# Performance work log

Hardware: AMD Instinct MI355X
Metric: run time of the kernel (lower is better)

## Reference

```python
import jax, jax.numpy as jnp
import numpy as np

NH = 12        # main attention heads (head_dim = 64)
SNH = 4        # scorer self-attention heads
ALPHA = 0.1    # static survival-score weight
EPS = 1e-8


def _linear(x, w, b):
    # torch nn.Linear: y = x @ W^T + b
    return x @ w.T + b


def _mha(x, in_w, in_b, out_w, out_b, n_heads, maskf):
    # torch nn.MultiheadAttention (batch_first, eval mode)
    B, S, D = x.shape
    hd = D // n_heads
    qkv = _linear(x, in_w, in_b)                      # [B,S,3D]
    q, k, v = jnp.split(qkv, 3, axis=-1)
    sp = lambda t: t.reshape(B, S, n_heads, hd).transpose(0, 2, 1, 3)
    q, k, v = sp(q), sp(k), sp(v)                     # [B,h,S,hd]
    scores = jnp.einsum('bhqd,bhkd->bhqk', q, k) / jnp.asarray(np.sqrt(hd), x.dtype)
    scores = jnp.where(maskf[:, None, None, :] > 0, scores, jnp.asarray(-1e9, x.dtype))
    aw = jax.nn.softmax(scores, axis=-1)
    o = jnp.einsum('bhqk,bhkd->bhqd', aw, v).transpose(0, 2, 1, 3).reshape(B, S, D)
    return _linear(o, out_w, out_b)


def _survival_scores(x, maskf, sp_w, sp_b, sa_in_w, sa_in_b, sa_out_w, sa_out_b,
                     nw1, nb1, nw2, nb2, mw1, mb1, mw2, mb2, dw1, db1, dw2, db2):
    h = _linear(x, sp_w, sp_b)                        # [B,S,256]
    h = _mha(h, sa_in_w, sa_in_b, sa_out_w, sa_out_b, SNH, maskf)
    n = jax.nn.softplus(_linear(jax.nn.relu(_linear(h, nw1, nb1)), nw2, nb2))[..., 0]
    mu = jax.nn.sigmoid(_linear(jax.nn.relu(_linear(h, mw1, mb1)), mw2, mb2))[..., 0]
    delta = jax.nn.relu(_linear(jax.nn.relu(_linear(h, dw1, db1)), dw2, db2))[..., 0]
    # S = log(N) + log(mu / mu_c) - delta, with mu_c = 1.0
    return jnp.log(n + EPS) + jnp.log(mu + EPS) - delta


def setup_inputs() -> dict:
    key = jax.random.key(0)
    ks = iter(jax.random.split(key, 40))
    W = lambda shape: jax.random.normal(next(ks), shape, jnp.float32) * 0.05
    Z = lambda shape: jnp.zeros(shape, jnp.float32)
    B, S, H, I = 2, 2048, 768, 256
    inp = {
        'x': jax.random.normal(next(ks), (B, S, H), jnp.float32),
        'mask': jnp.ones((B, S), jnp.int32),
        'qw': W((H, H)), 'qb': Z((H,)),
        'kw': W((H, H)), 'kb': Z((H,)),
        'vw': W((H, H)), 'vb': Z((H,)),
        'ow': W((H, H)), 'ob': Z((H,)),
        'sp_w': W((I, H)), 'sp_b': Z((I,)),
        'sa_in_w': W((3 * I, I)), 'sa_in_b': Z((3 * I,)),
        'sa_out_w': W((I, I)), 'sa_out_b': Z((I,)),
        'nw1': W((I // 2, I)), 'nb1': Z((I // 2,)), 'nw2': W((1, I // 2)), 'nb2': Z((1,)),
        'mw1': W((I // 2, I)), 'mb1': Z((I // 2,)), 'mw2': W((1, I // 2)), 'mb2': Z((1,)),
        'dw1': W((I // 2, I)), 'db1': Z((I // 2,)), 'dw2': W((1, I // 2)), 'db2': Z((1,)),
    }
    return inp


def reference(x, mask, qw, qb, kw, kb, vw, vb, ow, ob,
              sp_w, sp_b, sa_in_w, sa_in_b, sa_out_w, sa_out_b,
              nw1, nb1, nw2, nb2, mw1, mb1, mw2, mb2, dw1, db1, dw2, db2):
    B, S, H = x.shape
    hd = H // NH
    maskf = mask.astype(x.dtype)
    # Q/K/V projections -> [B,h,S,hd]
    sp = lambda t: t.reshape(B, S, NH, hd).transpose(0, 2, 1, 3)
    q = sp(_linear(x, qw, qb))
    k = sp(_linear(x, kw, kb))
    v = sp(_linear(x, vw, vb))
    scores = jnp.einsum('bhqd,bhkd->bhqk', q, k) / jnp.asarray(np.sqrt(hd), x.dtype)
    # survival-score bias (broadcast over heads and query positions)
    surv = _survival_scores(x, maskf, sp_w, sp_b, sa_in_w, sa_in_b, sa_out_w, sa_out_b,
                            nw1, nb1, nw2, nb2, mw1, mb1, mw2, mb2, dw1, db1, dw2, db2)
    scores = scores + ALPHA * surv[:, None, None, :]
    scores = scores + (1.0 - maskf)[:, None, None, :] * -1e9
    aw = jax.nn.softmax(scores, axis=-1)
    out = jnp.einsum('bhqk,bhkd->bhqd', aw, v).transpose(0, 2, 1, 3).reshape(B, S, H)
    return _linear(out, ow, ob)
```

## Files before the change

### kernel.cpp

```cpp
#include <hip/hip_runtime.h>
#include <math.h>

typedef __bf16 bf16;
typedef __bf16 bfrag __attribute__((ext_vector_type(8)));
typedef __bf16 bf4 __attribute__((ext_vector_type(4)));
typedef float f4 __attribute__((ext_vector_type(4)));
typedef float f16v __attribute__((ext_vector_type(16)));

#define LOG2E 1.4426950408889634f

#define DEV static __device__ __forceinline__

DEV f4 MFMA(bfrag a, bfrag b, f4 c) {
  return __builtin_amdgcn_mfma_f32_16x16x32_bf16(a, b, c, 0, 0, 0);
}
DEV f16v MFMA32(bfrag a, bfrag b, f16v c) {
  return __builtin_amdgcn_mfma_f32_32x32x16_bf16(a, b, c, 0, 0, 0);
}
DEV float ex2(float x) { return __builtin_amdgcn_exp2f(x); }
DEV unsigned pkbf(float a, float b) {
  bf16 ha = (bf16)a, hb = (bf16)b;
  unsigned short ua = __builtin_bit_cast(unsigned short, ha);
  unsigned short ub = __builtin_bit_cast(unsigned short, hb);
  return (unsigned)ua | ((unsigned)ub << 16);
}
DEV void gload_lds16(const bf16* g, bf16* l) {
  __builtin_amdgcn_global_load_lds(
      (const __attribute__((address_space(1))) void*)g,
      (__attribute__((address_space(3))) void*)l, 16, 0, 0);
}

__global__ __launch_bounds__(256) void pack_all(
    const float* __restrict__ x, const float* __restrict__ qw, const float* __restrict__ kw,
    const float* __restrict__ vw, const float* __restrict__ ow, const float* __restrict__ sp_w,
    const float* __restrict__ sa_in_w, const float* __restrict__ sa_out_w,
    const float* __restrict__ nw1, const float* __restrict__ mw1, const float* __restrict__ dw1,
    const float* __restrict__ qb, const float* __restrict__ kb, const float* __restrict__ vb,
    const float* __restrict__ nb1, const float* __restrict__ mb1, const float* __restrict__ db1,
    const int* __restrict__ mask,
    bf16* __restrict__ xb, bf16* __restrict__ wqkv, bf16* __restrict__ wob,
    bf16* __restrict__ spwb, bf16* __restrict__ sainb, bf16* __restrict__ saoutb,
    bf16* __restrict__ w1pack, float* __restrict__ bqkv, float* __restrict__ b1pack,
    float* __restrict__ maskBias) {
  int bid = blockIdx.x;
  int tid = threadIdx.x;
  const float* src = nullptr;
  bf16* dst = nullptr;
  int rel = 0;
  if (bid < 3072)      { src = x;       dst = xb;                   rel = bid; }
  else if (bid < 3648) { src = qw;      dst = wqkv;                 rel = bid - 3072; }
  else if (bid < 4224) { src = kw;      dst = wqkv + 589824;        rel = bid - 3648; }
  else if (bid < 4800) { src = vw;      dst = wqkv + 2 * 589824;    rel = bid - 4224; }
  else if (bid < 5376) { src = ow;      dst = wob;                  rel = bid - 4800; }
  else if (bid < 5568) { src = sp_w;    dst = spwb;                 rel = bid - 5376; }
  else if (bid < 5760) { src = sa_in_w; dst = sainb;                rel = bid - 5568; }
  else if (bid < 5824) { src = sa_out_w;dst = saoutb;               rel = bid - 5760; }
  else if (bid < 5856) { src = nw1;     dst = w1pack;               rel = bid - 5824; }
  else if (bid < 5888) { src = mw1;     dst = w1pack + 32768;       rel = bid - 5856; }
  else if (bid < 5920) { src = dw1;     dst = w1pack + 2 * 32768;   rel = bid - 5888; }
  else if (bid == 5920) {
    if (tid < 576) {
      int which = tid / 192, j = tid % 192;
      const float* s = which == 0 ? qb : (which == 1 ? kb : vb);
      reinterpret_cast<float4*>(bqkv)[tid] = reinterpret_cast<const float4*>(s)[j];
    }
    return;
  } else if (bid == 5921) {
    if (tid < 96) {
      int which = tid / 32, j = tid % 32;
      const float* s = which == 0 ? nb1 : (which == 1 ? mb1 : db1);
      reinterpret_cast<float4*>(b1pack)[tid] = reinterpret_cast<const float4*>(s)[j];
    }
    return;
  } else {
    int idx = (bid - 5922) * 256 + tid;
    int4 m = reinterpret_cast<const int4*>(mask)[idx];
    float4 o;
    o.x = m.x > 0 ? 0.f : -1e9f * LOG2E;
    o.y = m.y > 0 ? 0.f : -1e9f * LOG2E;
    o.z = m.z > 0 ? 0.f : -1e9f * LOG2E;
    o.w = m.w > 0 ? 0.f : -1e9f * LOG2E;
    reinterpret_cast<float4*>(maskBias)[idx] = o;
    return;
  }
  int i = rel * 256 + tid;
  float4 v = reinterpret_cast<const float4*>(src)[i];
  bf4 o;
  o[0] = (bf16)v.x; o[1] = (bf16)v.y; o[2] = (bf16)v.z; o[3] = (bf16)v.w;
  reinterpret_cast<bf4*>(dst)[i] = o;
}

template<int OUTF32, int RELU>
__global__ __launch_bounds__(256) void gemm_nt(
    const bf16* __restrict__ A, int lda,
    const bf16* __restrict__ W, int ldw,
    const float* __restrict__ bias,
    void* __restrict__ C, int ldc,
    int N64, int K) {
  int lane = threadIdx.x & 63;
  int w = threadIdx.x >> 6;
  int lrow = lane & 15, lgrp = lane >> 4;
  int tn = blockIdx.x % N64, tm = blockIdx.x / N64;
  int m0 = tm * 64 + (w >> 1) * 32;
  int n0 = tn * 64 + (w & 1) * 32;
  const bf16* Ab = A + (size_t)m0 * lda + lgrp * 8;
  const bf16* Wb = W + (size_t)n0 * ldw + lgrp * 8;
  f4 acc[2][2] = {};
  for (int k0 = 0; k0 < K; k0 += 32) {
    bfrag a0 = *(const bfrag*)(Ab + (size_t)lrow * lda + k0);
    bfrag a1 = *(const bfrag*)(Ab + (size_t)(lrow + 16) * lda + k0);
    bfrag b0 = *(const bfrag*)(Wb + (size_t)lrow * ldw + k0);
    bfrag b1 = *(const bfrag*)(Wb + (size_t)(lrow + 16) * ldw + k0);
    acc[0][0] = MFMA(a0, b0, acc[0][0]);
    acc[0][1] = MFMA(a0, b1, acc[0][1]);
    acc[1][0] = MFMA(a1, b0, acc[1][0]);
    acc[1][1] = MFMA(a1, b1, acc[1][1]);
  }
#pragma unroll
  for (int mi = 0; mi < 2; mi++)
#pragma unroll
    for (int nj = 0; nj < 2; nj++) {
      int col = n0 + nj * 16 + lrow;
      float bv = bias[col];
      int rowb = m0 + mi * 16 + lgrp * 4;
#pragma unroll
      for (int i = 0; i < 4; i++) {
        float v = acc[mi][nj][i] + bv;
        if (RELU) v = fmaxf(v, 0.f);
        if (OUTF32)
          ((float*)C)[(size_t)(rowb + i) * ldc + col] = v;
        else
          ((bf16*)C)[(size_t)(rowb + i) * ldc + col] = (bf16)v;
      }
    }
}

template<int OUTF32>
__global__ __launch_bounds__(256, 2) void gemm_big(
    const bf16* __restrict__ A,
    const bf16* __restrict__ W,
    const float* __restrict__ bias,
    void* __restrict__ C, int ldc,
    int N128, int K) {
  __shared__ char smem[65536];
  int lane = threadIdx.x & 63;
  int w = threadIdx.x >> 6;
  int lrow = lane & 15, lgrp = lane >> 4;
  int tn = blockIdx.x % N128, tm = blockIdx.x / N128;
  int m0 = tm * 128, n0 = tn * 128;

  int srow = lane >> 3;
  int sslot = (lane & 7) ^ srow;

  auto stage = [&](int bufb, int k0) {
#pragma unroll
    for (int j = 0; j < 4; j++) {
      int rb = (w * 4 + j) * 8 + srow;
      gload_lds16(A + (size_t)(m0 + rb) * K + k0 + sslot * 8,
                  (bf16*)(smem + bufb + (w * 4 + j) * 1024));
      gload_lds16(W + (size_t)(n0 + rb) * K + k0 + sslot * 8,
                  (bf16*)(smem + bufb + 16384 + (w * 4 + j) * 1024));
    }
  };

  f4 acc[4][4] = {};
  int swz = (lrow & 7) << 4;
  int mbase = (w >> 1) * 64, nbase = (w & 1) * 64;

  stage(0, 0);
  __syncthreads();
  int buf = 0;
  int nt = K / 64;
  for (int t = 0; t < nt; t++) {
    int nbuf = buf ^ 32768;
    if (t + 1 < nt) stage(nbuf, (t + 1) * 64);
    const char* As = smem + buf;
    const char* Ws = smem + buf + 16384;
#pragma unroll
    for (int kb = 0; kb < 128; kb += 64) {
      bfrag a[4], b[4];
#pragma unroll
      for (int i = 0; i < 4; i++) {
        a[i] = *(const bfrag*)(As + (mbase + i * 16 + lrow) * 128 + ((kb + lgrp * 16) ^ swz));
        b[i] = *(const bfrag*)(Ws + (nbase + i * 16 + lrow) * 128 + ((kb + lgrp * 16) ^ swz));
      }
#pragma unroll
      for (int mi = 0; mi < 4; mi++)
#pragma unroll
        for (int nj = 0; nj < 4; nj++)
          acc[mi][nj] = MFMA(a[mi], b[nj], acc[mi][nj]);
    }
    __syncthreads();
    buf = nbuf;
  }

#pragma unroll
  for (int mi = 0; mi < 4; mi++)
#pragma unroll
    for (int nj = 0; nj < 4; nj++) {
      int col = n0 + nbase + nj * 16 + lrow;
      float bv = bias[col];
      int rowb = m0 + mbase + mi * 16 + lgrp * 4;
#pragma unroll
      for (int i = 0; i < 4; i++) {
        float v = acc[mi][nj][i] + bv;
        if (OUTF32)
          ((float*)C)[(size_t)(rowb + i) * ldc + col] = v;
        else
          ((bf16*)C)[(size_t)(rowb + i) * ldc + col] = (bf16)v;
      }
    }
}

__global__ __launch_bounds__(256) void vtrans(const bf16* __restrict__ V, int rs, int coff,
                                              bf16* __restrict__ Vt, int H, int S) {
  int nst = S / 64;
  int st = blockIdx.x % nst;
  int h = (blockIdx.x / nst) % H;
  int b = blockIdx.x / (nst * H);
  __shared__ bf16 tile[64][72];
  int t = threadIdx.x;
  int r = t >> 2, c = t & 3;
  const bf16* src = V + ((size_t)b * S + st * 64 + r) * rs + coff + h * 64 + c * 16;
  bfrag v0 = *(const bfrag*)(src);
  bfrag v1 = *(const bfrag*)(src + 8);
  *(bfrag*)&tile[r][c * 16] = v0;
  *(bfrag*)&tile[r][c * 16 + 8] = v1;
  __syncthreads();
  bf16* dst = Vt + (((size_t)b * H + h) * 64 + r) * S + st * 64 + c * 16;
  bfrag o0, o1;
#pragma unroll
  for (int j = 0; j < 8; j++) {
    o0[j] = tile[c * 16 + j][r];
    o1[j] = tile[c * 16 + 8 + j][r];
  }
  *(bfrag*)dst = o0;
  *(bfrag*)(dst + 8) = o1;
}

template<int SPLIT, int PARTIAL>
__global__ __launch_bounds__(256) void flash6_k(
    const bf16* __restrict__ Q, const bf16* __restrict__ Kp, int rs,
    const bf16* __restrict__ Vt, const float* __restrict__ bias,
    bf16* __restrict__ O, int ors,
    float* __restrict__ Opart, float* __restrict__ Lpart,
    int H, int S, float scale, int Bc) {
  int nqt = S / 128;
  int bid = blockIdx.x;
  int qt = bid % nqt;
  int hh = (bid / nqt) % H;
  int b = (bid / (nqt * H)) % Bc;
  int sp = bid / (nqt * H * Bc);
  int lane = threadIdx.x & 63, w = threadIdx.x >> 6;
  int l31 = lane & 31, hf = lane >> 5;
  int q0 = qt * 128 + w * 32;
  const int kchunk = S / SPLIT;
  int k_beg = sp * kchunk;
  int swzl = (l31 & 7) << 4;

  const bf16* Qb = Q + ((size_t)b * S + q0 + l31) * rs + hh * 64 + hf * 8;
  bfrag qf[4];
#pragma unroll
  for (int c = 0; c < 4; c++) qf[c] = *(const bfrag*)(Qb + 16 * c);

  const bf16* gK0 = Kp + ((size_t)b * S + k_beg) * rs + hh * 64;
  const bf16* gV0 = Vt + (((size_t)b * H + hh) * 64) * (size_t)S + k_beg;
  const float* biasb = bias + (size_t)b * S;

  __shared__ bf16 KT[2][4096];
  __shared__ bf16 VT[2][4096];

  f16v acc0, acc1;
#pragma unroll
  for (int r = 0; r < 16; r++) { acc0[r] = 0.f; acc1[r] = 0.f; }
  float lrun = 0.f;

  int sidx0 = (w * 2) * 64 + lane;
  int sidx1 = (w * 2 + 1) * 64 + lane;
  int srow0 = sidx0 >> 3, sc0 = sidx0 & 7;
  int srow1 = sidx1 >> 3, sc1 = sidx1 & 7;
  int soff0 = srow0 * 128 + ((sc0 * 16) ^ ((srow0 & 7) << 4));
  int soff1 = srow1 * 128 + ((sc1 * 16) ^ ((srow1 & 7) << 4));

  bfrag kr0, kr1, vr0, vr1;
  kr0 = *(const bfrag*)(gK0 + (size_t)srow0 * rs + sc0 * 8);
  kr1 = *(const bfrag*)(gK0 + (size_t)srow1 * rs + sc1 * 8);
  vr0 = *(const bfrag*)(gV0 + (size_t)srow0 * S + sc0 * 8);
  vr1 = *(const bfrag*)(gV0 + (size_t)srow1 * S + sc1 * 8);
  *(bfrag*)((char*)KT[0] + soff0) = kr0;
  *(bfrag*)((char*)KT[0] + soff1) = kr1;
  *(bfrag*)((char*)VT[0] + soff0) = vr0;
  *(bfrag*)((char*)VT[0] + soff1) = vr1;
  __syncthreads();

  const int nt = kchunk / 64;
  for (int t = 0; t < nt; t++) {
    int kt = k_beg + t * 64;
    if (t + 1 < nt) {
      const bf16* gK = gK0 + (size_t)(t + 1) * 64 * rs;
      const bf16* gV = gV0 + (t + 1) * 64;
      kr0 = *(const bfrag*)(gK + (size_t)srow0 * rs + sc0 * 8);
      kr1 = *(const bfrag*)(gK + (size_t)srow1 * rs + sc1 * 8);
      vr0 = *(const bfrag*)(gV + (size_t)srow0 * S + sc0 * 8);
      vr1 = *(const bfrag*)(gV + (size_t)srow1 * S + sc1 * 8);
    }

    const char* KTb = (const char*)KT[t & 1];
    const char* VTb = (const char*)VT[t & 1];

    f16v s_lo, s_hi;
#pragma unroll
    for (int r = 0; r < 16; r++) { s_lo[r] = 0.f; s_hi[r] = 0.f; }
#pragma unroll
    for (int c = 0; c < 4; c++) {
      int colb = 32 * c + 16 * hf;
      bfrag klo = *(const bfrag*)(KTb + l31 * 128 + (colb ^ swzl));
      bfrag khi = *(const bfrag*)(KTb + (32 + l31) * 128 + (colb ^ swzl));
      s_lo = MFMA32(klo, qf[c], s_lo);
      s_hi = MFMA32(khi, qf[c], s_hi);
    }

    f4 blo[4], bhi[4];
#pragma unroll
    for (int g = 0; g < 4; g++) {
      blo[g] = *(const f4*)(biasb + kt + g * 8 + hf * 4);
      bhi[g] = *(const f4*)(biasb + kt + 32 + g * 8 + hf * 4);
    }
#pragma unroll
    for (int r = 0; r < 16; r++) {
      s_lo[r] = ex2(s_lo[r] * scale + blo[r >> 2][r & 3]);
      s_hi[r] = ex2(s_hi[r] * scale + bhi[r >> 2][r & 3]);
    }
    float rsum = s_lo[0] + s_hi[0];
#pragma unroll
    for (int r = 1; r < 16; r++) rsum += s_lo[r] + s_hi[r];
    rsum += __shfl_xor(rsum, 32);
    lrun += rsum;

    bfrag pb[4];
#pragma unroll
    for (int cc = 0; cc < 4; cc++) {
      const f16v& sv = (cc < 2) ? s_lo : s_hi;
      int rb = (cc & 1) * 8;
      unsigned lo0 = pkbf(sv[rb + 0], sv[rb + 1]);
      unsigned lo1 = pkbf(sv[rb + 2], sv[rb + 3]);
      unsigned hi0 = pkbf(sv[rb + 4], sv[rb + 5]);
      unsigned hi1 = pkbf(sv[rb + 6], sv[rb + 7]);
      unsigned t0 = hf ? lo0 : hi0;
      unsigned t1 = hf ? lo1 : hi1;
      unsigned r0 = (unsigned)__shfl_xor((int)t0, 32);
      unsigned r1 = (unsigned)__shfl_xor((int)t1, 32);
      union { bfrag v; unsigned u[4]; } pu;
      pu.u[0] = hf ? r0 : lo0;
      pu.u[1] = hf ? r1 : lo1;
      pu.u[2] = hf ? hi0 : r0;
      pu.u[3] = hf ? hi1 : r1;
      pb[cc] = pu.v;
    }

#pragma unroll
    for (int c = 0; c < 4; c++) {
      int colb = 32 * c + 16 * hf;
      bfrag v0 = *(const bfrag*)(VTb + l31 * 128 + (colb ^ swzl));
      bfrag v1 = *(const bfrag*)(VTb + (32 + l31) * 128 + (colb ^ swzl));
      acc0 = MFMA32(v0, pb[c], acc0);
      acc1 = MFMA32(v1, pb[c], acc1);
    }

    if (t + 1 < nt) {
      char* KTn = (char*)KT[(t + 1) & 1];
      char* VTn = (char*)VT[(t + 1) & 1];
      *(bfrag*)(KTn + soff0) = kr0;
      *(bfrag*)(KTn + soff1) = kr1;
      *(bfrag*)(VTn + soff0) = vr0;
      *(bfrag*)(VTn + soff1) = vr1;
    }
    __syncthreads();
  }

  int q = q0 + l31;
  if (PARTIAL) {
    float* op = Opart + ((((size_t)sp * Bc + b) * H + hh) * S + q) * 64 + hf * 4;
#pragma unroll
    for (int g = 0; g < 4; g++) {
      f4 v0, v1;
#pragma unroll
      for (int i = 0; i < 4; i++) { v0[i] = acc0[4 * g + i]; v1[i] = acc1[4 * g + i]; }
      *(f4*)(op + g * 8) = v0;
      *(f4*)(op + 32 + g * 8) = v1;
    }
    if (hf == 0)
      Lpart[(((size_t)sp * Bc + b) * H + hh) * S + q] = lrun;
  } else {
    float inv = 1.f / lrun;
    bf16* Ob = O + ((size_t)b * S + q) * ors + hh * 64 + hf * 4;
#pragma unroll
    for (int g = 0; g < 4; g++) {
      bf4 o0, o1;
#pragma unroll
      for (int i = 0; i < 4; i++) {
        o0[i] = (bf16)(acc0[4 * g + i] * inv);
        o1[i] = (bf16)(acc1[4 * g + i] * inv);
      }
      *(bf4*)(Ob + g * 8) = o0;
      *(bf4*)(Ob + 32 + g * 8) = o1;
    }
  }
}

__global__ __launch_bounds__(256) void flash_comb(
    const float* __restrict__ Opart, const float* __restrict__ L,
    bf16* __restrict__ O, int ors, int Hh, int S, int Bc, int nsplit) {
  int idx = blockIdx.x * 256 + threadIdx.x;
  int d4 = idx & 15;
  int q = (idx >> 4) % S;
  int hh = ((idx >> 4) / S) % Hh;
  int b = (idx >> 4) / (S * Hh);
  size_t rowstride = (size_t)Bc * Hh * S;
  size_t rbase = ((size_t)b * Hh + hh) * S + q;
  float lsum = 0.f;
  f4 o = {0.f, 0.f, 0.f, 0.f};
  for (int sp = 0; sp < nsplit; sp++) {
    lsum += L[sp * rowstride + rbase];
    f4 a = *(const f4*)(Opart + (sp * rowstride + rbase) * 64 + d4 * 4);
#pragma unroll
    for (int i = 0; i < 4; i++) o[i] += a[i];
  }
  float inv = 1.f / lsum;
  bf4 obv;
#pragma unroll
  for (int i = 0; i < 4; i++) obv[i] = (bf16)(o[i] * inv);
  *(bf4*)(O + ((size_t)b * S + q) * ors + hh * 64 + d4 * 4) = obv;
}

__global__ __launch_bounds__(256) void surv_k(
    const bf16* __restrict__ hid,
    const float* __restrict__ nw2, const float* __restrict__ nb2,
    const float* __restrict__ mw2, const float* __restrict__ mb2,
    const float* __restrict__ dw2, const float* __restrict__ db2,
    const float* __restrict__ maskBias, float* __restrict__ biasMain) {
  int w = threadIdx.x >> 6, lane = threadIdx.x & 63;
  int row = blockIdx.x * 4 + w;
  const bf16* hr = hid + (size_t)row * 384;
  const float* W2[3] = {nw2, mw2, dw2};
  float outs[3];
#pragma unroll
  for (int t = 0; t < 3; t++) {
    float acc = (float)hr[t * 128 + lane] * W2[t][lane] +
                (float)hr[t * 128 + 64 + lane] * W2[t][64 + lane];
    for (int msk = 1; msk < 64; msk <<= 1) acc += __shfl_xor(acc, msk);
    outs[t] = acc;
  }
  if (lane == 0) {
    float xn = outs[0] + nb2[0];
    float n = (xn > 20.f) ? xn : log1pf(__expf(xn));
    float mu = 1.f / (1.f + __expf(-(outs[1] + mb2[0])));
    float delta = fmaxf(outs[2] + db2[0], 0.f);
    float surv = logf(n + 1e-8f) + logf(mu + 1e-8f) - delta;
    biasMain[row] = 0.1f * LOG2E * surv + maskBias[row];
  }
}

extern "C" void kernel_launch(void* const* d_in, const int* in_sizes, int n_in,
                              void* d_out, int out_size, void* d_ws, size_t ws_size,
                              hipStream_t stream) {
  const int B = 2, S = 2048, H = 768, I = 256;
  const int NH = 12, SNH = 4;
  const int M = B * S;
  const float SC = 0.125f * LOG2E;

  const float* x = (const float*)d_in[0];
  const int* mask = (const int*)d_in[1];
  const float* qw = (const float*)d_in[2];
  const float* qb = (const float*)d_in[3];
  const float* kw = (const float*)d_in[4];
  const float* kb = (const float*)d_in[5];
  const float* vw = (const float*)d_in[6];
  const float* vb = (const float*)d_in[7];
  const float* ow = (const float*)d_in[8];
  const float* ob = (const float*)d_in[9];
  const float* sp_w = (const float*)d_in[10];
  const float* sp_b = (const float*)d_in[11];
  const float* sa_in_w = (const float*)d_in[12];
  const float* sa_in_b = (const float*)d_in[13];
  const float* sa_out_w = (const float*)d_in[14];
  const float* sa_out_b = (const float*)d_in[15];
  const float* nw1 = (const float*)d_in[16];
  const float* nb1 = (const float*)d_in[17];
  const float* nw2 = (const float*)d_in[18];
  const float* nb2 = (const float*)d_in[19];
  const float* mw1 = (const float*)d_in[20];
  const float* mb1 = (const float*)d_in[21];
  const float* mw2 = (const float*)d_in[22];
  const float* mb2 = (const float*)d_in[23];
  const float* dw1 = (const float*)d_in[24];
  const float* db1 = (const float*)d_in[25];
  const float* dw2 = (const float*)d_in[26];
  const float* db2 = (const float*)d_in[27];

  char* ws = (char*)d_ws;
  size_t off = 0;
  auto alloc = [&](size_t bytes) -> void* {
    void* p = ws + off;
    off += (bytes + 255) & ~(size_t)255;
    return p;
  };

  bf16* xb = (bf16*)alloc((size_t)M * H * 2);
  bf16* wqkv = (bf16*)alloc((size_t)3 * H * H * 2);
  float* bqkv = (float*)alloc((size_t)3 * H * 4);
  bf16* wob = (bf16*)alloc((size_t)H * H * 2);
  bf16* spwb = (bf16*)alloc((size_t)I * H * 2);
  bf16* sainb = (bf16*)alloc((size_t)(3 * I) * I * 2);
  bf16* saoutb = (bf16*)alloc((size_t)I * I * 2);
  bf16* w1pack = (bf16*)alloc((size_t)384 * 256 * 2);
  float* b1pack = (float*)alloc((size_t)384 * 4);
  float* maskBias = (float*)alloc((size_t)M * 4);
  float* biasMain = (float*)alloc((size_t)M * 4);

  const int SPM = 4, SPS = 8;
  size_t offMark = off;
  bf16* h0 = (bf16*)alloc((size_t)M * I * 2);
  bf16* qkv_s = (bf16*)alloc((size_t)M * (3 * I) * 2);
  bf16* vt_s = (bf16*)alloc((size_t)B * SNH * 64 * S * 2);
  bf16* attn_s = (bf16*)alloc((size_t)M * I * 2);
  bf16* h1 = (bf16*)alloc((size_t)M * I * 2);
  bf16* hid = (bf16*)alloc((size_t)M * 384 * 2);
  float* Opart_s = (float*)alloc((size_t)SPS * B * SNH * S * 64 * 4);
  float* L_s = (float*)alloc((size_t)SPS * B * SNH * S * 4);
  size_t endA = off;
  off = offMark;
  bf16* QKVm = (bf16*)alloc((size_t)M * 3 * H * 2);
  bf16* vt_m = (bf16*)alloc((size_t)B * NH * 64 * S * 2);
  bf16* attn_m = (bf16*)alloc((size_t)M * H * 2);
  float* Opart_m = (float*)alloc((size_t)SPM * B * NH * S * 64 * 4);
  float* L_m = (float*)alloc((size_t)SPM * B * NH * S * 4);
  size_t endB = off;
  size_t need = endA > endB ? endA : endB;
  bool split_ok = ws_size >= need;
  (void)in_sizes; (void)n_in; (void)out_size;

  pack_all<<<5926, 256, 0, stream>>>(x, qw, kw, vw, ow, sp_w, sa_in_w, sa_out_w, nw1, mw1, dw1,
                                     qb, kb, vb, nb1, mb1, db1, mask,
                                     xb, wqkv, wob, spwb, sainb, saoutb, w1pack, bqkv, b1pack,
                                     maskBias);

  gemm_nt<0, 0><<<(M / 64) * (I / 64), 256, 0, stream>>>(xb, H, spwb, H, sp_b, h0, I, I / 64, H);
  gemm_nt<0, 0><<<(M / 64) * ((3 * I) / 64), 256, 0, stream>>>(h0, I, sainb, I, sa_in_b, qkv_s,
                                                               3 * I, (3 * I) / 64, I);
  vtrans<<<B * SNH * (S / 64), 256, 0, stream>>>(qkv_s, 3 * I, 2 * I, vt_s, SNH, S);
  if (split_ok) {
    flash6_k<SPS, 1><<<SPS * B * SNH * (S / 128), 256, 0, stream>>>(
        qkv_s, qkv_s + I, 3 * I, vt_s, maskBias, nullptr, 0, Opart_s, L_s, SNH, S, SC, B);
    flash_comb<<<(B * SNH * S * 16) / 256, 256, 0, stream>>>(Opart_s, L_s, attn_s, I, SNH, S,
                                                             B, SPS);
  } else {
    flash6_k<1, 0><<<B * SNH * (S / 128), 256, 0, stream>>>(
        qkv_s, qkv_s + I, 3 * I, vt_s, maskBias, attn_s, I, nullptr, nullptr, SNH, S, SC, B);
  }
  gemm_nt<0, 0><<<(M / 64) * (I / 64), 256, 0, stream>>>(attn_s, I, saoutb, I, sa_out_b, h1, I,
                                                         I / 64, I);
  gemm_nt<0, 1><<<(M / 64) * (384 / 64), 256, 0, stream>>>(h1, I, w1pack, I, b1pack, hid, 384,
                                                           384 / 64, I);
  surv_k<<<M / 4, 256, 0, stream>>>(hid, nw2, nb2, mw2, mb2, dw2, db2, maskBias, biasMain);

  gemm_big<0><<<(M / 128) * (3 * H / 128), 256, 0, stream>>>(xb, wqkv, bqkv, QKVm, 3 * H,
                                                             3 * H / 128, H);
  vtrans<<<B * NH * (S / 64), 256, 0, stream>>>(QKVm, 3 * H, 2 * H, vt_m, NH, S);
  if (split_ok) {
    flash6_k<SPM, 1><<<SPM * B * NH * (S / 128), 256, 0, stream>>>(
        QKVm, QKVm + H, 3 * H, vt_m, biasMain, nullptr, 0, Opart_m, L_m, NH, S, SC, B);
    flash_comb<<<(B * NH * S * 16) / 256, 256, 0, stream>>>(Opart_m, L_m, attn_m, H, NH, S, B,
                                                            SPM);
  } else {
    flash6_k<1, 0><<<B * NH * (S / 128), 256, 0, stream>>>(
        QKVm, QKVm + H, 3 * H, vt_m, biasMain, attn_m, H, nullptr, nullptr, NH, S, SC, B);
  }
  gemm_big<1><<<(M / 128) * (H / 128), 256, 0, stream>>>(attn_m, wob, ob, d_out, H,
                                                         H / 128, H);
}
```

Measured before the change: 211.6 us.

## Stage K/V tiles with direct global-to-LDS loads and halve split-K factor

```diff
diff --git a/kernel.cpp b/kernel.cpp
--- a/kernel.cpp
+++ b/kernel.cpp
@@ -239,7 +239,7 @@
 }
 
 template<int SPLIT, int PARTIAL>
-__global__ __launch_bounds__(256) void flash6_k(
+__global__ __launch_bounds__(256) void flash7_k(
     const bf16* __restrict__ Q, const bf16* __restrict__ Kp, int rs,
     const bf16* __restrict__ Vt, const float* __restrict__ bias,
     bf16* __restrict__ O, int ors,
@@ -275,38 +275,31 @@
   for (int r = 0; r < 16; r++) { acc0[r] = 0.f; acc1[r] = 0.f; }
   float lrun = 0.f;
 
-  int sidx0 = (w * 2) * 64 + lane;
-  int sidx1 = (w * 2 + 1) * 64 + lane;
-  int srow0 = sidx0 >> 3, sc0 = sidx0 & 7;
-  int srow1 = sidx1 >> 3, sc1 = sidx1 & 7;
-  int soff0 = srow0 * 128 + ((sc0 * 16) ^ ((srow0 & 7) << 4));
-  int soff1 = srow1 * 128 + ((sc1 * 16) ^ ((srow1 & 7) << 4));
-
-  bfrag kr0, kr1, vr0, vr1;
-  kr0 = *(const bfrag*)(gK0 + (size_t)srow0 * rs + sc0 * 8);
-  kr1 = *(const bfrag*)(gK0 + (size_t)srow1 * rs + sc1 * 8);
-  vr0 = *(const bfrag*)(gV0 + (size_t)srow0 * S + sc0 * 8);
-  vr1 = *(const bfrag*)(gV0 + (size_t)srow1 * S + sc1 * 8);
-  *(bfrag*)((char*)KT[0] + soff0) = kr0;
-  *(bfrag*)((char*)KT[0] + soff1) = kr1;
-  *(bfrag*)((char*)VT[0] + soff0) = vr0;
-  *(bfrag*)((char*)VT[0] + soff1) = vr1;
+  int srow = lane >> 3;
+  int sel = ((lane & 7) ^ srow) * 8;
+  int r0 = (w * 2) * 8 + srow;
+  int r1 = (w * 2 + 1) * 8 + srow;
+
+  auto stage = [&](int bb, int kt) {
+    const bf16* gK = gK0 + (size_t)(kt - k_beg) * rs;
+    const bf16* gV = gV0 + (kt - k_beg);
+    gload_lds16(gK + (size_t)r0 * rs + sel, KT[bb] + (w * 2) * 512);
+    gload_lds16(gK + (size_t)r1 * rs + sel, KT[bb] + (w * 2 + 1) * 512);
+    gload_lds16(gV + (size_t)r0 * S + sel, VT[bb] + (w * 2) * 512);
+    gload_lds16(gV + (size_t)r1 * S + sel, VT[bb] + (w * 2 + 1) * 512);
+  };
+
+  stage(0, k_beg);
   __syncthreads();
 
   const int nt = kchunk / 64;
+  int buf = 0;
   for (int t = 0; t < nt; t++) {
     int kt = k_beg + t * 64;
-    if (t + 1 < nt) {
-      const bf16* gK = gK0 + (size_t)(t + 1) * 64 * rs;
-      const bf16* gV = gV0 + (t + 1) * 64;
-      kr0 = *(const bfrag*)(gK + (size_t)srow0 * rs + sc0 * 8);
-      kr1 = *(const bfrag*)(gK + (size_t)srow1 * rs + sc1 * 8);
-      vr0 = *(const bfrag*)(gV + (size_t)srow0 * S + sc0 * 8);
-      vr1 = *(const bfrag*)(gV + (size_t)srow1 * S + sc1 * 8);
-    }
-
-    const char* KTb = (const char*)KT[t & 1];
-    const char* VTb = (const char*)VT[t & 1];
+    if (t + 1 < nt) stage(buf ^ 1, kt + 64);
+
+    const char* KTb = (const char*)KT[buf];
+    const char* VTb = (const char*)VT[buf];
 
     f16v s_lo, s_hi;
 #pragma unroll
@@ -348,13 +341,13 @@
       unsigned hi1 = pkbf(sv[rb + 6], sv[rb + 7]);
       unsigned t0 = hf ? lo0 : hi0;
       unsigned t1 = hf ? lo1 : hi1;
-      unsigned r0 = (unsigned)__shfl_xor((int)t0, 32);
-      unsigned r1 = (unsigned)__shfl_xor((int)t1, 32);
+      unsigned r0s = (unsigned)__shfl_xor((int)t0, 32);
+      unsigned r1s = (unsigned)__shfl_xor((int)t1, 32);
       union { bfrag v; unsigned u[4]; } pu;
-      pu.u[0] = hf ? r0 : lo0;
-      pu.u[1] = hf ? r1 : lo1;
-      pu.u[2] = hf ? hi0 : r0;
-      pu.u[3] = hf ? hi1 : r1;
+      pu.u[0] = hf ? r0s : lo0;
+      pu.u[1] = hf ? r1s : lo1;
+      pu.u[2] = hf ? hi0 : r0s;
+      pu.u[3] = hf ? hi1 : r1s;
       pb[cc] = pu.v;
     }
 
@@ -367,15 +360,8 @@
       acc1 = MFMA32(v1, pb[c], acc1);
     }
 
-    if (t + 1 < nt) {
-      char* KTn = (char*)KT[(t + 1) & 1];
-      char* VTn = (char*)VT[(t + 1) & 1];
-      *(bfrag*)(KTn + soff0) = kr0;
-      *(bfrag*)(KTn + soff1) = kr1;
-      *(bfrag*)(VTn + soff0) = vr0;
-      *(bfrag*)(VTn + soff1) = vr1;
-    }
     __syncthreads();
+    buf ^= 1;
   }
 
   int q = q0 + l31;
@@ -518,7 +504,7 @@
   float* maskBias = (float*)alloc((size_t)M * 4);
   float* biasMain = (float*)alloc((size_t)M * 4);
 
-  const int SPM = 4, SPS = 8;
+  const int SPM = 2, SPS = 4;
   size_t offMark = off;
   bf16* h0 = (bf16*)alloc((size_t)M * I * 2);
   bf16* qkv_s = (bf16*)alloc((size_t)M * (3 * I) * 2);
@@ -550,12 +536,12 @@
                                                                3 * I, (3 * I) / 64, I);
   vtrans<<<B * SNH * (S / 64), 256, 0, stream>>>(qkv_s, 3 * I, 2 * I, vt_s, SNH, S);
   if (split_ok) {
-    flash6_k<SPS, 1><<<SPS * B * SNH * (S / 128), 256, 0, stream>>>(
+    flash7_k<SPS, 1><<<SPS * B * SNH * (S / 128), 256, 0, stream>>>(
         qkv_s, qkv_s + I, 3 * I, vt_s, maskBias, nullptr, 0, Opart_s, L_s, SNH, S, SC, B);
     flash_comb<<<(B * SNH * S * 16) / 256, 256, 0, stream>>>(Opart_s, L_s, attn_s, I, SNH, S,
                                                              B, SPS);
   } else {
-    flash6_k<1, 0><<<B * SNH * (S / 128), 256, 0, stream>>>(
+    flash7_k<1, 0><<<B * SNH * (S / 128), 256, 0, stream>>>(
         qkv_s, qkv_s + I, 3 * I, vt_s, maskBias, attn_s, I, nullptr, nullptr, SNH, S, SC, B);
   }
   gemm_nt<0, 0><<<(M / 64) * (I / 64), 256, 0, stream>>>(attn_s, I, saoutb, I, sa_out_b, h1, I,
@@ -568,12 +554,12 @@
                                                              3 * H / 128, H);
   vtrans<<<B * NH * (S / 64), 256, 0, stream>>>(QKVm, 3 * H, 2 * H, vt_m, NH, S);
   if (split_ok) {
-    flash6_k<SPM, 1><<<SPM * B * NH * (S / 128), 256, 0, stream>>>(
+    flash7_k<SPM, 1><<<SPM * B * NH * (S / 128), 256, 0, stream>>>(
         QKVm, QKVm + H, 3 * H, vt_m, biasMain, nullptr, 0, Opart_m, L_m, NH, S, SC, B);
     flash_comb<<<(B * NH * S * 16) / 256, 256, 0, stream>>>(Opart_m, L_m, attn_m, H, NH, S, B,
                                                             SPM);
   } else {
-    flash6_k<1, 0><<<B * NH * (S / 128), 256, 0, stream>>>(
+    flash7_k<1, 0><<<B * NH * (S / 128), 256, 0, stream>>>(
         QKVm, QKVm + H, 3 * H, vt_m, biasMain, attn_m, H, nullptr, nullptr, NH, S, SC, B);
   }
   gemm_big<1><<<(M / 128) * (H / 128), 256, 0, stream>>>(attn_m, wob, ob, d_out, H,
```

New measurement: 196.8 us. 1.07x faster.
